# Performance work log

Hardware: AMD Instinct MI355X
Metric: run time of the kernel (lower is better)

## Reference

```python
import jax, jax.numpy as jnp
import numpy as np

D_MODEL = 1024
N_HEAD = 16
D_HEAD = D_MODEL // N_HEAD
EXP = 4
B, T = 2, 2048
EPS = 1e-5

def setup_inputs() -> dict:
    key = jax.random.key(0)
    ks = jax.random.split(key, 16)
    s = 0.02
    return {
        "x": jax.random.normal(ks[0], (B, T, D_MODEL), jnp.float32),
        "ln1_w": jnp.ones((D_MODEL,), jnp.float32),
        "ln1_b": jnp.zeros((D_MODEL,), jnp.float32),
        "attn_w": jax.random.normal(ks[1], (D_MODEL, 3 * D_MODEL), jnp.float32) * s,
        "attn_b": jnp.zeros((3 * D_MODEL,), jnp.float32),
        "proj_w": jax.random.normal(ks[2], (D_MODEL, D_MODEL), jnp.float32) * s,
        "proj_b": jnp.zeros((D_MODEL,), jnp.float32),
        "ln2_w": jnp.ones((D_MODEL,), jnp.float32),
        "ln2_b": jnp.zeros((D_MODEL,), jnp.float32),
        "fc_w": jax.random.normal(ks[3], (D_MODEL, EXP * D_MODEL), jnp.float32) * s,
        "fc_b": jnp.zeros((EXP * D_MODEL,), jnp.float32),
        "fc2_w": jax.random.normal(ks[4], (EXP * D_MODEL, D_MODEL), jnp.float32) * s,
        "fc2_b": jnp.zeros((D_MODEL,), jnp.float32),
    }

def _layernorm(x, w, b):
    mu = jnp.mean(x, axis=-1, keepdims=True)
    var = jnp.mean(jnp.square(x - mu), axis=-1, keepdims=True)
    return (x - mu) * jax.lax.rsqrt(var + EPS) * w + b

def _attn(x, attn_w, attn_b, proj_w, proj_b):
    Bx, Tx, C = x.shape
    qkv = x @ attn_w + attn_b  # [B,T,3C]
    q, k, v = jnp.split(qkv, 3, axis=-1)
    # [B, H, T, Dh]
    q = q.reshape(Bx, Tx, N_HEAD, D_HEAD).transpose(0, 2, 1, 3)
    k = k.reshape(Bx, Tx, N_HEAD, D_HEAD).transpose(0, 2, 1, 3)
    v = v.reshape(Bx, Tx, N_HEAD, D_HEAD).transpose(0, 2, 1, 3)
    att = jnp.einsum('bhqd,bhkd->bhqk', q, k) * (1.0 / np.sqrt(D_HEAD))
    causal = jnp.tril(jnp.ones((Tx, Tx), bool))
    att = jnp.where(causal, att, -jnp.inf)
    att = jax.nn.softmax(att, axis=-1)
    y = jnp.einsum('bhqk,bhkd->bhqd', att, v)
    y = y.transpose(0, 2, 1, 3).reshape(Bx, Tx, C)
    return y @ proj_w + proj_b

def reference(x, ln1_w, ln1_b, attn_w, attn_b, proj_w, proj_b,
              ln2_w, ln2_b, fc_w, fc_b, fc2_w, fc2_b):
    x = x + _attn(_layernorm(x, ln1_w, ln1_b), attn_w, attn_b, proj_w, proj_b)
    h = _layernorm(x, ln2_w, ln2_b)
    h = jax.nn.gelu(h @ fc_w + fc_b, approximate=False)  # exact GELU (torch nn.GELU default)
    x = x + (h @ fc2_w + fc2_b)
    return x
```

## Files before the change

### kernel.cpp

```cpp
#include <hip/hip_runtime.h>
#include <hip/hip_bf16.h>
#include <math.h>


#define D_MODEL 1024
#define N_HEAD  16
#define D_HEAD  64
#define SEQ_T   2048
#define BATCH   2
#define NROWS   (BATCH * SEQ_T)
#define C3      (3 * D_MODEL)
#define D_FF    (4 * D_MODEL)

typedef __bf16 bf16x8 __attribute__((ext_vector_type(8)));
typedef __bf16 bf16x4t __attribute__((ext_vector_type(4)));
typedef short  s16x4  __attribute__((ext_vector_type(4)));
typedef float  f32x4  __attribute__((ext_vector_type(4)));

#define WAIT_VM0() asm volatile("s_waitcnt vmcnt(0)" ::: "memory")
#define WAIT_VM2() asm volatile("s_waitcnt vmcnt(2)" ::: "memory")
#define WAIT_VM4() asm volatile("s_waitcnt vmcnt(4)" ::: "memory")
#define WAIT_VM6() asm volatile("s_waitcnt vmcnt(6)" ::: "memory")

__device__ __forceinline__ f32x4 mfma16_bf16(s16x4 a, s16x4 b, f32x4 c)
{
#if __has_builtin(__builtin_amdgcn_mfma_f32_16x16x16_bf16)
    return __builtin_amdgcn_mfma_f32_16x16x16_bf16(
        __builtin_bit_cast(bf16x4t, a), __builtin_bit_cast(bf16x4t, b), c, 0, 0, 0);
#else
    return __builtin_amdgcn_mfma_f32_16x16x16bf16_1k(a, b, c, 0, 0, 0);
#endif
}

__global__ __launch_bounds__(256) void ln_kernel(
    const float* __restrict__ in, const float* __restrict__ w,
    const float* __restrict__ b, __hip_bfloat16* __restrict__ out, int D)
{
    const int row = blockIdx.x;
    const int tid = threadIdx.x;
    const float* x = in + (size_t)row * 1024;

    const float4 v = *(const float4*)(x + tid * 4);
    float s  = v.x + v.y + v.z + v.w;
    float s2 = v.x * v.x + v.y * v.y + v.z * v.z + v.w * v.w;

    __shared__ float rs[256], rs2[256];
    rs[tid] = s; rs2[tid] = s2;
    __syncthreads();
    for (int off = 128; off > 0; off >>= 1) {
        if (tid < off) { rs[tid] += rs[tid + off]; rs2[tid] += rs2[tid + off]; }
        __syncthreads();
    }
    const float mu   = rs[0] * (1.0f / 1024.0f);
    const float var  = rs2[0] * (1.0f / 1024.0f) - mu * mu;
    const float rstd = rsqrtf(var + 1e-5f);

    const float4 w4 = *(const float4*)(w + tid * 4);
    const float4 b4 = *(const float4*)(b + tid * 4);
    float o[4] = {(v.x - mu) * rstd * w4.x + b4.x,
                  (v.y - mu) * rstd * w4.y + b4.y,
                  (v.z - mu) * rstd * w4.z + b4.z,
                  (v.w - mu) * rstd * w4.w + b4.w};
    ushort4 pk;
    { __hip_bfloat16 e0 = __float2bfloat16(o[0]); pk.x = *(unsigned short*)&e0;
      __hip_bfloat16 e1 = __float2bfloat16(o[1]); pk.y = *(unsigned short*)&e1;
      __hip_bfloat16 e2 = __float2bfloat16(o[2]); pk.z = *(unsigned short*)&e2;
      __hip_bfloat16 e3 = __float2bfloat16(o[3]); pk.w = *(unsigned short*)&e3; }
    *(ushort4*)(out + (size_t)row * 1024 + tid * 4) = pk;
}

__global__ __launch_bounds__(256) void prep_kernel(
    const float* __restrict__ attn_w, const float* __restrict__ proj_w,
    const float* __restrict__ fc_w,   const float* __restrict__ fc2_w,
    __hip_bfloat16* __restrict__ attn_wt, __hip_bfloat16* __restrict__ proj_wt,
    __hip_bfloat16* __restrict__ fc_wt,   __hip_bfloat16* __restrict__ fc2_wt,
    const float* __restrict__ x, const float* __restrict__ ln1_w,
    const float* __restrict__ ln1_b, __hip_bfloat16* __restrict__ ln_out)
{
    __shared__ float smem[32 * 33];
    int tb = blockIdx.x;
    const int tid = threadIdx.x;

    if (tb >= 12288) {
        const int row = tb - 12288;
        const float* xr = x + (size_t)row * 1024;
        const float4 v = *(const float4*)(xr + tid * 4);
        float s  = v.x + v.y + v.z + v.w;
        float s2 = v.x * v.x + v.y * v.y + v.z * v.z + v.w * v.w;
        float* rs  = smem;
        float* rs2 = smem + 256;
        rs[tid] = s; rs2[tid] = s2;
        __syncthreads();
        for (int off = 128; off > 0; off >>= 1) {
            if (tid < off) { rs[tid] += rs[tid + off]; rs2[tid] += rs2[tid + off]; }
            __syncthreads();
        }
        const float mu   = rs[0] * (1.0f / 1024.0f);
        const float var  = rs2[0] * (1.0f / 1024.0f) - mu * mu;
        const float rstd = rsqrtf(var + 1e-5f);
        const float4 w4 = *(const float4*)(ln1_w + tid * 4);
        const float4 b4 = *(const float4*)(ln1_b + tid * 4);
        float o[4] = {(v.x - mu) * rstd * w4.x + b4.x,
                      (v.y - mu) * rstd * w4.y + b4.y,
                      (v.z - mu) * rstd * w4.z + b4.z,
                      (v.w - mu) * rstd * w4.w + b4.w};
        ushort4 pk;
        { __hip_bfloat16 e0 = __float2bfloat16(o[0]); pk.x = *(unsigned short*)&e0;
          __hip_bfloat16 e1 = __float2bfloat16(o[1]); pk.y = *(unsigned short*)&e1;
          __hip_bfloat16 e2 = __float2bfloat16(o[2]); pk.z = *(unsigned short*)&e2;
          __hip_bfloat16 e3 = __float2bfloat16(o[3]); pk.w = *(unsigned short*)&e3; }
        *(ushort4*)(ln_out + (size_t)row * 1024 + tid * 4) = pk;
        return;
    }

    float (*t)[33] = (float(*)[33])smem;
    const float* W; __hip_bfloat16* Wt; int K, N;
    if (tb < 3072)      { W = attn_w; Wt = attn_wt; K = D_MODEL; N = C3; }
    else if (tb < 4096) { tb -= 3072; W = proj_w; Wt = proj_wt; K = D_MODEL; N = D_MODEL; }
    else if (tb < 8192) { tb -= 4096; W = fc_w;   Wt = fc_wt;   K = D_MODEL; N = D_FF; }
    else                { tb -= 8192; W = fc2_w;  Wt = fc2_wt;  K = D_FF;    N = D_MODEL; }
    const int ntx = N >> 5;
    const int k0 = (tb / ntx) * 32;
    const int n0 = (tb % ntx) * 32;

    const int row = tid >> 3;
    const int c4  = (tid & 7) * 4;

    const float4 v = *(const float4*)&W[(size_t)(k0 + row) * N + n0 + c4];
    t[row][c4 + 0] = v.x; t[row][c4 + 1] = v.y;
    t[row][c4 + 2] = v.z; t[row][c4 + 3] = v.w;
    __syncthreads();

    ushort4 pk;
    { __hip_bfloat16 e0 = __float2bfloat16(t[c4 + 0][row]); pk.x = *(unsigned short*)&e0;
      __hip_bfloat16 e1 = __float2bfloat16(t[c4 + 1][row]); pk.y = *(unsigned short*)&e1;
      __hip_bfloat16 e2 = __float2bfloat16(t[c4 + 2][row]); pk.z = *(unsigned short*)&e2;
      __hip_bfloat16 e3 = __float2bfloat16(t[c4 + 3][row]); pk.w = *(unsigned short*)&e3; }
    *(ushort4*)&Wt[(size_t)(n0 + row) * K + k0 + c4] = pk;
}

__device__ __forceinline__ void async16(const __hip_bfloat16* g, __hip_bfloat16* l)
{
    __builtin_amdgcn_global_load_lds(
        (const __attribute__((address_space(1))) void*)g,
        (__attribute__((address_space(3))) void*)l, 16, 0, 0);
}

__device__ __forceinline__ float gelu_fast(float v)
{
    const float t = v * (0.7978845608f + 0.0356774081f * v * v);
    return v / (1.0f + exp2f(-2.885390082f * t));
}

__device__ __forceinline__ void swz_xcd(int& bx, int& by)
{
    const int nbx = gridDim.x;
    const int nwg = nbx * gridDim.y;
    int lin = blockIdx.y * nbx + blockIdx.x;
    const int per = nwg >> 3;
    lin = (lin & 7) * per + (lin >> 3);
    bx = lin % nbx;
    by = lin / nbx;
}


__device__ __forceinline__ void gemm8p_core(
    const __hip_bfloat16* __restrict__ A,
    const __hip_bfloat16* __restrict__ Bt,
    int K, int row0, int col0, f32x4 (&acc)[8][4],
    __hip_bfloat16 (*Asl)[4][64 * 64], __hip_bfloat16 (*Bsl)[2][128 * 64])
{
    const int tid  = threadIdx.x;
    const int wv   = tid >> 6;
    const int lane = tid & 63;
    const int ln15 = lane & 15;
    const int lq   = lane >> 4;
    const int wr   = wv >> 2;
    const int wc   = wv & 3;

    const int srow = tid >> 3;
    const int sg   = ((tid & 7) ^ ((tid >> 3) & 7)) * 8;
    const __hip_bfloat16* Ab = A  + (size_t)(row0 + srow) * K + sg;
    const __hip_bfloat16* Bb = Bt + (size_t)(col0 + srow) * K + sg;
    const int nt = K >> 6;

#pragma unroll
    for (int mi = 0; mi < 8; ++mi)
#pragma unroll
        for (int ni = 0; ni < 4; ++ni) acc[mi][ni] = (f32x4){0.f, 0.f, 0.f, 0.f};

    auto stA = [&](int t, int buf, int b) {
        async16(Ab + (size_t)(b * 64) * K + t * 64, &Asl[buf][b][0] + tid * 8);
    };
    auto stB = [&](int t, int buf, int h) {
        async16(Bb + (size_t)(h * 128) * K + t * 64, &Bsl[buf][h][0] + tid * 8);
        async16(Bb + (size_t)(h * 128 + 64) * K + t * 64,
                &Bsl[buf][h][0] + 4096 + tid * 8);
    };

    const int rg0 = (lq ^ (ln15 & 7)) * 8;
    const int rg1 = ((4 | lq) ^ (ln15 & 7)) * 8;
    auto ldA = [&](int buf, int mi, int kk) -> bf16x8 {
        return *(const bf16x8*)&Asl[buf][wr * 2 + (mi >> 2)]
            [((mi & 3) * 16 + ln15) * 64 + (kk ? rg1 : rg0)];
    };
    auto ldB = [&](int buf, int ni, int kk) -> bf16x8 {
        return *(const bf16x8*)&Bsl[buf][wc >> 1]
            [((wc & 1) * 64 + ni * 16 + ln15) * 64 + (kk ? rg1 : rg0)];
    };

    stB(0, 0, 0); stB(0, 0, 1);
    stA(0, 0, 0); stA(0, 0, 2); stA(0, 0, 1); stA(0, 0, 3);
    WAIT_VM0();
    __builtin_amdgcn_s_barrier();

    for (int t = 0; t < nt; ++t) {
        const int pp = t & 1, op = pp ^ 1;
        const int tc = (t + 1 < nt) ? t + 1 : nt - 1;
        bf16x8 af[2][2], bfr[4][2];

#pragma unroll
        for (int m = 0; m < 2; ++m) { af[m][0] = ldA(pp, m, 0); af[m][1] = ldA(pp, m, 1); }
#pragma unroll
        for (int ni = 0; ni < 4; ++ni) { bfr[ni][0] = ldB(pp, ni, 0); bfr[ni][1] = ldB(pp, ni, 1); }
        stB(tc, op, 0);
        __builtin_amdgcn_s_barrier();
        __builtin_amdgcn_s_setprio(1);
#pragma unroll
        for (int kk = 0; kk < 2; ++kk)
#pragma unroll
            for (int m = 0; m < 2; ++m)
#pragma unroll
                for (int ni = 0; ni < 4; ++ni)
                    acc[m][ni] = __builtin_amdgcn_mfma_f32_16x16x32_bf16(
                        af[m][kk], bfr[ni][kk], acc[m][ni], 0, 0, 0);
        __builtin_amdgcn_s_setprio(0);
        __builtin_amdgcn_s_barrier();

#pragma unroll
        for (int m = 0; m < 2; ++m) { af[m][0] = ldA(pp, 2 + m, 0); af[m][1] = ldA(pp, 2 + m, 1); }
        stB(tc, op, 1);
        WAIT_VM4();
        __builtin_amdgcn_s_barrier();
        __builtin_amdgcn_s_setprio(1);
#pragma unroll
        for (int kk = 0; kk < 2; ++kk)
#pragma unroll
            for (int m = 0; m < 2; ++m)
#pragma unroll
                for (int ni = 0; ni < 4; ++ni)
                    acc[2 + m][ni] = __builtin_amdgcn_mfma_f32_16x16x32_bf16(
                        af[m][kk], bfr[ni][kk], acc[2 + m][ni], 0, 0, 0);
        __builtin_amdgcn_s_setprio(0);
        __builtin_amdgcn_s_barrier();

#pragma unroll
        for (int m = 0; m < 2; ++m) { af[m][0] = ldA(pp, 4 + m, 0); af[m][1] = ldA(pp, 4 + m, 1); }
        stA(tc, op, 0); stA(tc, op, 2);
        __builtin_amdgcn_s_barrier();
        __builtin_amdgcn_s_setprio(1);
#pragma unroll
        for (int kk = 0; kk < 2; ++kk)
#pragma unroll
            for (int m = 0; m < 2; ++m)
#pragma unroll
                for (int ni = 0; ni < 4; ++ni)
                    acc[4 + m][ni] = __builtin_amdgcn_mfma_f32_16x16x32_bf16(
                        af[m][kk], bfr[ni][kk], acc[4 + m][ni], 0, 0, 0);
        __builtin_amdgcn_s_setprio(0);
        __builtin_amdgcn_s_barrier();

#pragma unroll
        for (int m = 0; m < 2; ++m) { af[m][0] = ldA(pp, 6 + m, 0); af[m][1] = ldA(pp, 6 + m, 1); }
        stA(tc, op, 1); stA(tc, op, 3);
        WAIT_VM2();
        __builtin_amdgcn_s_barrier();
        __builtin_amdgcn_s_setprio(1);
#pragma unroll
        for (int kk = 0; kk < 2; ++kk)
#pragma unroll
            for (int m = 0; m < 2; ++m)
#pragma unroll
                for (int ni = 0; ni < 4; ++ni)
                    acc[6 + m][ni] = __builtin_amdgcn_mfma_f32_16x16x32_bf16(
                        af[m][kk], bfr[ni][kk], acc[6 + m][ni], 0, 0, 0);
        __builtin_amdgcn_s_setprio(0);
        __builtin_amdgcn_s_barrier();
    }
}

__global__ __launch_bounds__(512, 1) void gemm8p_kernel(
    const __hip_bfloat16* __restrict__ A,
    const __hip_bfloat16* __restrict__ Bt,
    const float* __restrict__ bias,
    __hip_bfloat16* __restrict__ Cout,
    int M, int N, int K, int act)
{
    __shared__ __align__(16) __hip_bfloat16 Asl[2][4][64 * 64];
    __shared__ __align__(16) __hip_bfloat16 Bsl[2][2][128 * 64];

    int bx, by;
    swz_xcd(bx, by);
    const int row0 = by * 256;
    const int col0 = bx * 256;

    f32x4 acc[8][4];
    gemm8p_core(A, Bt, K, row0, col0, acc, Asl, Bsl);

    const int tid  = threadIdx.x;
    const int wv   = tid >> 6;
    const int lane = tid & 63;
    const int ln15 = lane & 15;
    const int lq   = lane >> 4;
    const int mbase = (wv >> 2) * 128;
    const int nbase = (wv & 3) * 64;

#pragma unroll
    for (int mi = 0; mi < 8; ++mi) {
#pragma unroll
        for (int ni = 0; ni < 4; ++ni) {
            const int gc = col0 + nbase + ni * 16 + ln15;
            const float bv = bias[gc];
#pragma unroll
            for (int r = 0; r < 4; ++r) {
                const int gr = row0 + mbase + mi * 16 + lq * 4 + r;
                float v = acc[mi][ni][r] + bv;
                if (act == 1) v = gelu_fast(v);
                Cout[(size_t)gr * N + gc] = __float2bfloat16(v);
            }
        }
    }
}

__global__ __launch_bounds__(512, 1) void qkv8p_kernel(
    const __hip_bfloat16* __restrict__ A,
    const __hip_bfloat16* __restrict__ Bt,
    const float* __restrict__ bias,
    __hip_bfloat16* __restrict__ Qb,
    __hip_bfloat16* __restrict__ Kb,
    __hip_bfloat16* __restrict__ Vtb)
{
    __shared__ __align__(16) __hip_bfloat16 Asl[2][4][64 * 64];
    __shared__ __align__(16) __hip_bfloat16 Bsl[2][2][128 * 64];

    int bx, by;
    swz_xcd(bx, by);
    const int row0 = by * 256;
    const int col0 = bx * 256;

    f32x4 acc[8][4];
    gemm8p_core(A, Bt, D_MODEL, row0, col0, acc, Asl, Bsl);

    const int tid  = threadIdx.x;
    const int wv   = tid >> 6;
    const int lane = tid & 63;
    const int ln15 = lane & 15;
    const int lq   = lane >> 4;
    const int mbase = (wv >> 2) * 128;
    const int nbase = (wv & 3) * 64;

#pragma unroll
    for (int mi = 0; mi < 8; ++mi) {
        const int gr0 = row0 + mbase + mi * 16 + lq * 4;
        const int bb  = gr0 >> 11;
        const int q0  = gr0 & 2047;
#pragma unroll
        for (int ni = 0; ni < 4; ++ni) {
            const int gc  = col0 + nbase + ni * 16 + ln15;
            const float bv = bias[gc];
            const int sec = gc >> 10;
            const int hd  = (gc & 1023) >> 6;
            const int d   = gc & 63;
            if (sec == 2) {
                unsigned short u[4];
#pragma unroll
                for (int r = 0; r < 4; ++r) {
                    __hip_bfloat16 e = __float2bfloat16(acc[mi][ni][r] + bv);
                    u[r] = *(unsigned short*)&e;
                }
                uint2 pk;
                pk.x = (unsigned int)u[0] | ((unsigned int)u[1] << 16);
                pk.y = (unsigned int)u[2] | ((unsigned int)u[3] << 16);
                *(uint2*)(Vtb + ((size_t)((bb * N_HEAD + hd) * D_HEAD + d)) * SEQ_T + q0) = pk;
            } else {
                __hip_bfloat16* dst = (sec == 0 ? Qb : Kb)
                    + ((size_t)((bb * N_HEAD + hd) * SEQ_T + q0)) * D_HEAD + d;
#pragma unroll
                for (int r = 0; r < 4; ++r)
                    dst[(size_t)r * D_HEAD] = __float2bfloat16(acc[mi][ni][r] + bv);
            }
        }
    }
}

__device__ __forceinline__ void stage_db2w(
    const __hip_bfloat16* __restrict__ Ab, const __hip_bfloat16* __restrict__ Bb,
    int K, int kt, __hip_bfloat16* __restrict__ as,
    __hip_bfloat16* __restrict__ bs, int tid)
{
    const int k0 = kt * 64;
#pragma unroll
    for (int s = 0; s < 2; ++s) {
        async16(Ab + k0 + s * 32, as + s * 64 * 32 + tid * 8);
#pragma unroll
        for (int i = 0; i < 2; ++i)
            async16(Bb + (size_t)(i * 64) * K + k0 + s * 32,
                    bs + s * 128 * 32 + i * 64 * 32 + tid * 8);
    }
}

__device__ __forceinline__ void gemm_db2w(
    const __hip_bfloat16* __restrict__ A,
    const __hip_bfloat16* __restrict__ Bt,
    int K, int row0, int col0, f32x4 (&acc)[2][4])
{
    __shared__ __align__(16) __hip_bfloat16 Asl[3][2 * 64 * 32];
    __shared__ __align__(16) __hip_bfloat16 Bsl[3][2 * 128 * 32];

    const int tid  = threadIdx.x;
    const int wv   = tid >> 6;
    const int lane = tid & 63;
    const int ln15 = lane & 15;
    const int lq   = lane >> 4;
    const int mbase = (wv >> 1) * 32;
    const int nbase = (wv & 1) * 64;
    const int rcol = (lq ^ ((ln15 >> 1) & 3)) * 8;
    const int ssw  = ((tid & 3) ^ ((tid >> 3) & 3)) * 8;
    const __hip_bfloat16* Ab = A  + (size_t)(row0 + (tid >> 2)) * K + ssw;
    const __hip_bfloat16* Bb = Bt + (size_t)(col0 + (tid >> 2)) * K + ssw;
    const int nt = K >> 6;

#pragma unroll
    for (int mi = 0; mi < 2; ++mi)
#pragma unroll
        for (int ni = 0; ni < 4; ++ni) acc[mi][ni] = (f32x4){0.f, 0.f, 0.f, 0.f};

    stage_db2w(Ab, Bb, K, 0, &Asl[0][0], &Bsl[0][0], tid);
    stage_db2w(Ab, Bb, K, 1, &Asl[1][0], &Bsl[1][0], tid);
    WAIT_VM6();
    __builtin_amdgcn_s_barrier();

    for (int t = 0; t < nt; ++t) {
        const int p   = t % 3;
        const int p2  = (t + 2) % 3;
        const int tcl = (t + 2 < nt) ? t + 2 : nt - 1;
        bf16x8 af[2][2], bfr[2][4];

#pragma unroll
        for (int s = 0; s < 2; ++s) {
#pragma unroll
            for (int mi = 0; mi < 2; ++mi)
                af[s][mi] = *(const bf16x8*)
                    &Asl[p][s * 64 * 32 + (mbase + mi * 16 + ln15) * 32 + rcol];
#pragma unroll
            for (int ni = 0; ni < 4; ++ni)
                bfr[s][ni] = *(const bf16x8*)
                    &Bsl[p][s * 128 * 32 + (nbase + ni * 16 + ln15) * 32 + rcol];
        }

        stage_db2w(Ab, Bb, K, tcl, &Asl[p2][0], &Bsl[p2][0], tid);

        WAIT_VM6();
        __builtin_amdgcn_s_barrier();

        __builtin_amdgcn_s_setprio(1);
#pragma unroll
        for (int s = 0; s < 2; ++s)
#pragma unroll
            for (int mi = 0; mi < 2; ++mi)
#pragma unroll
                for (int ni = 0; ni < 4; ++ni)
                    acc[mi][ni] = __builtin_amdgcn_mfma_f32_16x16x32_bf16(
                        af[s][mi], bfr[s][ni], acc[mi][ni], 0, 0, 0);
        __builtin_amdgcn_s_setprio(0);
    }
}

__global__ __launch_bounds__(256, 2) void gemm64_kernel(
    const __hip_bfloat16* __restrict__ A,
    const __hip_bfloat16* __restrict__ Bt,
    const float* __restrict__ bias,
    const float* __restrict__ residual,
    void* __restrict__ Cout,
    int M, int N, int K, int act, int outBf16)
{
    int bx, by;
    swz_xcd(bx, by);
    const int row0 = by * 64;
    const int col0 = bx * 128;

    f32x4 acc[2][4];
    gemm_db2w(A, Bt, K, row0, col0, acc);

    const int tid  = threadIdx.x;
    const int wv   = tid >> 6;
    const int lane = tid & 63;
    const int ln15 = lane & 15;
    const int lq   = lane >> 4;
    const int mbase = (wv >> 1) * 32;
    const int nbase = (wv & 1) * 64;

#pragma unroll
    for (int mi = 0; mi < 2; ++mi) {
#pragma unroll
        for (int ni = 0; ni < 4; ++ni) {
            const int gc = col0 + nbase + ni * 16 + ln15;
            const float bv = bias[gc];
#pragma unroll
            for (int r = 0; r < 4; ++r) {
                const int gr = row0 + mbase + mi * 16 + lq * 4 + r;
                float v = acc[mi][ni][r] + bv;
                if (act == 1) v = gelu_fast(v);
                if (residual) v += residual[(size_t)gr * N + gc];
                if (outBf16)
                    ((__hip_bfloat16*)Cout)[(size_t)gr * N + gc] = __float2bfloat16(v);
                else
                    ((float*)Cout)[(size_t)gr * N + gc] = v;
            }
        }
    }
}

#define ATQ 64
#define ATK 128
#define NQT (SEQ_T / ATQ)
#define VP2 136

__global__ __launch_bounds__(256) void mfma_attn_kernel(
    const __hip_bfloat16* __restrict__ Qb,
    const __hip_bfloat16* __restrict__ Kb,
    const __hip_bfloat16* __restrict__ Vtb,
    __hip_bfloat16* __restrict__ y)
{
    __shared__ __align__(16) __hip_bfloat16 Ks[2][ATK * 64];
    __shared__ __align__(16) __hip_bfloat16 Vts[2][D_HEAD * VP2];

    const int flat = (blockIdx.z * gridDim.y + blockIdx.y) * gridDim.x + blockIdx.x;
    const int xcd  = flat & 7;
    const int slot = flat >> 3;
    const int pair = slot & 15;
    const int hb   = slot >> 4;
    const int h    = xcd + 8 * (hb & 1);
    const int b    = hb >> 1;

    const int tid  = threadIdx.x;
    const int wv   = tid >> 6;
    const int lane = tid & 63;
    const int ln15 = lane & 15;
    const int lq   = lane >> 4;

    const __hip_bfloat16* Qh = Qb  + (size_t)(b * N_HEAD + h) * SEQ_T * D_HEAD;
    const __hip_bfloat16* Kh = Kb  + (size_t)(b * N_HEAD + h) * SEQ_T * D_HEAD;
    const __hip_bfloat16* Vh = Vtb + (size_t)(b * N_HEAD + h) * D_HEAD * SEQ_T;
    const size_t bT = (size_t)b * SEQ_T;

    const float CEXP = 0.18033688011f;
    const float DTHR = 8.0f / CEXP;

    const int kr  = tid >> 3, kg = tid & 7;
    const int ksg = (kg ^ (kr & 7)) * 8;
    bf16x8 vreg[4];
    const int vr = tid >> 4, vc = tid & 15;

    auto issueK = [&](int kb, int buf) {
#pragma unroll
        for (int i = 0; i < 4; ++i)
            async16(Kh + (size_t)(kb + kr + i * 32) * D_HEAD + ksg,
                    &Ks[buf][i * 2048] + tid * 8);
    };
    auto issueV = [&](int kb) {
#pragma unroll
        for (int i = 0; i < 4; ++i)
            vreg[i] = *(const bf16x8*)(Vh + (size_t)(vr + i * 16) * SEQ_T + kb + vc * 8);
    };
    auto commitV = [&](int buf) {
#pragma unroll
        for (int i = 0; i < 4; ++i)
            *(bf16x8*)&Vts[buf][(vr + i * 16) * VP2 + vc * 8] = vreg[i];
    };

    const int rg0 = (lq ^ (ln15 & 7)) * 8;
    const int rg1 = ((4 | lq) ^ (ln15 & 7)) * 8;

#pragma unroll 1
    for (int half = 0; half < 2; ++half) {
        const int qt    = half == 0 ? pair : (NQT - 1 - pair);
        const int qbase = qt * ATQ;
        const int ntk   = (qt >> 1) + 1;
        const int qg    = qbase + wv * 16 + ln15;

        bf16x8 qf[2];
#pragma unroll
        for (int kc = 0; kc < 2; ++kc)
            qf[kc] = *(const bf16x8*)(Qh + (size_t)(qbase + wv * 16 + ln15) * D_HEAD
                                      + kc * 32 + lq * 8);

        f32x4 Oacc[4];
#pragma unroll
        for (int dn = 0; dn < 4; ++dn) Oacc[dn] = (f32x4){0.f, 0.f, 0.f, 0.f};
        float m_run = -INFINITY, l_run = 0.f;

        issueK(0, 0);
        issueV(0);

        for (int t = 0; t < ntk; ++t) {
            const int kb  = t * ATK;
            const int buf = t & 1;
            commitV(buf);
            __syncthreads();
            if (t + 1 < ntk) {
                issueK((t + 1) * ATK, buf ^ 1);
                issueV((t + 1) * ATK);
            }

            f32x4 st[8];
#pragma unroll
            for (int jf = 0; jf < 8; ++jf) st[jf] = (f32x4){0.f, 0.f, 0.f, 0.f};
            __builtin_amdgcn_s_setprio(1);
#pragma unroll
            for (int jf = 0; jf < 8; ++jf) {
                const int rw = jf * 16 + ln15;
                const bf16x8 kf0 = *(const bf16x8*)&Ks[buf][rw * 64 + rg0];
                const bf16x8 kf1 = *(const bf16x8*)&Ks[buf][rw * 64 + rg1];
                st[jf] = __builtin_amdgcn_mfma_f32_16x16x32_bf16(kf0, qf[0], st[jf], 0, 0, 0);
                st[jf] = __builtin_amdgcn_mfma_f32_16x16x32_bf16(kf1, qf[1], st[jf], 0, 0, 0);
            }
            __builtin_amdgcn_s_setprio(0);

            if (t == ntk - 1) {
#pragma unroll
                for (int jf = 0; jf < 8; ++jf)
#pragma unroll
                    for (int r = 0; r < 4; ++r)
                        if ((kb + jf * 16 + lq * 4 + r) > qg) st[jf][r] = -INFINITY;
            }

            float tm0 = st[0][0], tm1 = st[0][1], tm2 = st[0][2], tm3 = st[0][3];
#pragma unroll
            for (int jf = 1; jf < 8; ++jf) {
                tm0 = fmaxf(tm0, st[jf][0]);
                tm1 = fmaxf(tm1, st[jf][1]);
                tm2 = fmaxf(tm2, st[jf][2]);
                tm3 = fmaxf(tm3, st[jf][3]);
            }
            float tmax = fmaxf(fmaxf(tm0, tm1), fmaxf(tm2, tm3));
            tmax = fmaxf(tmax, __shfl_xor(tmax, 16));
            tmax = fmaxf(tmax, __shfl_xor(tmax, 32));

            if (!__all(tmax <= m_run + DTHR)) {
                const float mnew  = fmaxf(m_run, tmax);
                const float alpha = exp2f((m_run - mnew) * CEXP);
                l_run *= alpha;
                m_run = mnew;
                float a4[4];
#pragma unroll
                for (int r = 0; r < 4; ++r) a4[r] = __shfl(alpha, lq * 4 + r);
#pragma unroll
                for (int dn = 0; dn < 4; ++dn)
#pragma unroll
                    for (int r = 0; r < 4; ++r) Oacc[dn][r] *= a4[r];
            }
            const float mc = m_run * CEXP;
            float ps0 = 0.f, ps1 = 0.f, ps2 = 0.f, ps3 = 0.f;
#pragma unroll
            for (int jf = 0; jf < 8; ++jf) {
                const float p0 = exp2f(fmaf(st[jf][0], CEXP, -mc));
                const float p1 = exp2f(fmaf(st[jf][1], CEXP, -mc));
                const float p2 = exp2f(fmaf(st[jf][2], CEXP, -mc));
                const float p3 = exp2f(fmaf(st[jf][3], CEXP, -mc));
                st[jf][0] = p0; st[jf][1] = p1; st[jf][2] = p2; st[jf][3] = p3;
                ps0 += p0; ps1 += p1; ps2 += p2; ps3 += p3;
            }
            float psum = (ps0 + ps1) + (ps2 + ps3);
            psum += __shfl_xor(psum, 16);
            psum += __shfl_xor(psum, 32);
            l_run += psum;

            __builtin_amdgcn_s_setprio(1);
#pragma unroll
            for (int jf = 0; jf < 8; ++jf) {
                s16x4 pfr;
#pragma unroll
                for (int s = 0; s < 4; ++s) {
                    __hip_bfloat16 e = __float2bfloat16(st[jf][s]);
                    pfr[s] = __builtin_bit_cast(short, e);
                }
#pragma unroll
                for (int dn = 0; dn < 4; ++dn) {
                    const s16x4 vfr = *(const s16x4*)&Vts[buf][(dn * 16 + ln15) * VP2
                                                            + jf * 16 + lq * 4];
                    Oacc[dn] = mfma16_bf16(pfr, vfr, Oacc[dn]);
                }
            }
            __builtin_amdgcn_s_setprio(0);
        }

        __syncthreads();
        float il[4];
#pragma unroll
        for (int r = 0; r < 4; ++r) il[r] = 1.0f / __shfl(l_run, lq * 4 + r);
#pragma unroll
        for (int dn = 0; dn < 4; ++dn)
#pragma unroll
            for (int r = 0; r < 4; ++r)
                Ks[0][(wv * 16 + lq * 4 + r) * 72 + dn * 16 + ln15] =
                    __float2bfloat16(Oacc[dn][r] * il[r]);
        __syncthreads();
        const int r2 = lane >> 3, c8 = (lane & 7) * 8;
#pragma unroll
        for (int i = 0; i < 2; ++i) {
            const int row = wv * 16 + r2 + 8 * i;
            const bf16x8 val = *(const bf16x8*)&Ks[0][row * 72 + c8];
            *(bf16x8*)(y + (bT + qbase + row) * D_MODEL + h * D_HEAD + c8) = val;
        }
        __syncthreads();
    }
}

extern "C" void kernel_launch(void* const* d_in, const int* in_sizes, int n_in,
                              void* d_out, int out_size, void* d_ws, size_t ws_size,
                              hipStream_t stream)
{
    const float* x      = (const float*)d_in[0];
    const float* ln1_w  = (const float*)d_in[1];
    const float* ln1_b  = (const float*)d_in[2];
    const float* attn_w = (const float*)d_in[3];
    const float* attn_b = (const float*)d_in[4];
    const float* proj_w = (const float*)d_in[5];
    const float* proj_b = (const float*)d_in[6];
    const float* ln2_w  = (const float*)d_in[7];
    const float* ln2_b  = (const float*)d_in[8];
    const float* fc_w   = (const float*)d_in[9];
    const float* fc_b   = (const float*)d_in[10];
    const float* fc2_w  = (const float*)d_in[11];
    const float* fc2_b  = (const float*)d_in[12];
    float* out = (float*)d_out;

    char* ws = (char*)d_ws;
    __hip_bfloat16* Qb      = (__hip_bfloat16*)(ws);
    __hip_bfloat16* Kb      = (__hip_bfloat16*)(ws + (size_t)8  * 1024 * 1024);
    __hip_bfloat16* Vtb     = (__hip_bfloat16*)(ws + (size_t)16 * 1024 * 1024);
    __hip_bfloat16* h_bf    = (__hip_bfloat16*)(ws);
    __hip_bfloat16* ln_buf  = (__hip_bfloat16*)(ws + (size_t)32 * 1024 * 1024);
    __hip_bfloat16* y_buf   = (__hip_bfloat16*)(ws + (size_t)40 * 1024 * 1024);
    float*          xmid    = (float*)(ws + (size_t)48 * 1024 * 1024);
    __hip_bfloat16* attn_wt = (__hip_bfloat16*)(ws + (size_t)64 * 1024 * 1024);
    __hip_bfloat16* proj_wt = (__hip_bfloat16*)(ws + (size_t)70 * 1024 * 1024);
    __hip_bfloat16* fc_wt   = (__hip_bfloat16*)(ws + (size_t)72 * 1024 * 1024);
    __hip_bfloat16* fc2_wt  = (__hip_bfloat16*)(ws + (size_t)80 * 1024 * 1024);

    dim3 blk256(256);
    dim3 blk512(512);

    prep_kernel<<<dim3(12288 + NROWS), blk256, 0, stream>>>(
        attn_w, proj_w, fc_w, fc2_w, attn_wt, proj_wt, fc_wt, fc2_wt,
        x, ln1_w, ln1_b, ln_buf);

    qkv8p_kernel<<<dim3(C3 / 256, NROWS / 256), blk512, 0, stream>>>(
        ln_buf, attn_wt, attn_b, Qb, Kb, Vtb);

    mfma_attn_kernel<<<dim3(NQT / 2, N_HEAD, BATCH), blk256, 0, stream>>>(
        Qb, Kb, Vtb, y_buf);

    gemm64_kernel<<<dim3(D_MODEL / 128, NROWS / 64), blk256, 0, stream>>>(
        y_buf, proj_wt, proj_b, x, xmid, NROWS, D_MODEL, D_MODEL, 0, 0);

    ln_kernel<<<dim3(NROWS), blk256, 0, stream>>>(xmid, ln2_w, ln2_b, ln_buf, D_MODEL);

    gemm8p_kernel<<<dim3(D_FF / 256, NROWS / 256), blk512, 0, stream>>>(
        ln_buf, fc_wt, fc_b, h_bf, NROWS, D_FF, D_MODEL, 1);

    gemm64_kernel<<<dim3(D_MODEL / 128, NROWS / 64), blk256, 0, stream>>>(
        h_bf, fc2_wt, fc2_b, xmid, out, NROWS, D_MODEL, D_FF, 0, 0);
}
```

Baseline: 334.8 us.

## Process both paired causal query tiles concurrently in one 512-thread attention block

The attention kernel previously handled its two paired query tiles (a short one and a long one) one after the other with 256 threads. It now uses 512 threads, where the first 256 take the short tile and the second 256 take the long tile. Both groups share one K/V stream out of shared memory, and the short group simply idles once its keys run out. This halves the K/V loads per pair and doubles the parallelism per block, but the short-tile warps idle during the later iterations and the larger block may reduce occupancy.

Result: slower. 349.9 us (+4.5%).

```diff
diff --git a/kernel.cpp b/kernel.cpp
--- a/kernel.cpp
+++ b/kernel.cpp
@@ -526,7 +526,7 @@
 #define NQT (SEQ_T / ATQ)
 #define VP2 136
 
-__global__ __launch_bounds__(256) void mfma_attn_kernel(
+__global__ __launch_bounds__(512, 2) void mfma_attn_kernel(
     const __hip_bfloat16* __restrict__ Qb,
     const __hip_bfloat16* __restrict__ Kb,
     const __hip_bfloat16* __restrict__ Vtb,
@@ -544,7 +544,8 @@
     const int b    = hb >> 1;
 
     const int tid  = threadIdx.x;
-    const int wv   = tid >> 6;
+    const int wq   = tid >> 8;
+    const int wv4  = (tid >> 6) & 3;
     const int lane = tid & 63;
     const int ln15 = lane & 15;
     const int lq   = lane >> 4;
@@ -557,62 +558,61 @@
     const float CEXP = 0.18033688011f;
     const float DTHR = 8.0f / CEXP;
 
-    const int kr  = tid >> 3, kg = tid & 7;
-    const int ksg = (kg ^ (kr & 7)) * 8;
-    bf16x8 vreg[4];
+    const int qt_me  = (wq == 0) ? pair : (NQT - 1 - pair);
+    const int qbase  = qt_me * ATQ;
+    const int ntk_me = (qt_me >> 1) + 1;
+    const int ntkMax = ((NQT - 1 - pair) >> 1) + 1;
+    const int qg     = qbase + wv4 * 16 + ln15;
+
+    const int ksg = ((tid & 7) ^ ((tid >> 3) & 7)) * 8;
+    bf16x8 vreg[2];
     const int vr = tid >> 4, vc = tid & 15;
 
     auto issueK = [&](int kb, int buf) {
 #pragma unroll
-        for (int i = 0; i < 4; ++i)
-            async16(Kh + (size_t)(kb + kr + i * 32) * D_HEAD + ksg,
-                    &Ks[buf][i * 2048] + tid * 8);
+        for (int i = 0; i < 2; ++i)
+            async16(Kh + (size_t)(kb + (tid >> 3) + i * 64) * D_HEAD + ksg,
+                    &Ks[buf][i * 4096] + tid * 8);
     };
     auto issueV = [&](int kb) {
 #pragma unroll
-        for (int i = 0; i < 4; ++i)
-            vreg[i] = *(const bf16x8*)(Vh + (size_t)(vr + i * 16) * SEQ_T + kb + vc * 8);
+        for (int i = 0; i < 2; ++i)
+            vreg[i] = *(const bf16x8*)(Vh + (size_t)(vr + i * 32) * SEQ_T + kb + vc * 8);
     };
     auto commitV = [&](int buf) {
 #pragma unroll
-        for (int i = 0; i < 4; ++i)
-            *(bf16x8*)&Vts[buf][(vr + i * 16) * VP2 + vc * 8] = vreg[i];
+        for (int i = 0; i < 2; ++i)
+            *(bf16x8*)&Vts[buf][(vr + i * 32) * VP2 + vc * 8] = vreg[i];
     };
 
     const int rg0 = (lq ^ (ln15 & 7)) * 8;
     const int rg1 = ((4 | lq) ^ (ln15 & 7)) * 8;
 
-#pragma unroll 1
-    for (int half = 0; half < 2; ++half) {
-        const int qt    = half == 0 ? pair : (NQT - 1 - pair);
-        const int qbase = qt * ATQ;
-        const int ntk   = (qt >> 1) + 1;
-        const int qg    = qbase + wv * 16 + ln15;
-
-        bf16x8 qf[2];
-#pragma unroll
-        for (int kc = 0; kc < 2; ++kc)
-            qf[kc] = *(const bf16x8*)(Qh + (size_t)(qbase + wv * 16 + ln15) * D_HEAD
-                                      + kc * 32 + lq * 8);
-
-        f32x4 Oacc[4];
-#pragma unroll
-        for (int dn = 0; dn < 4; ++dn) Oacc[dn] = (f32x4){0.f, 0.f, 0.f, 0.f};
-        float m_run = -INFINITY, l_run = 0.f;
-
-        issueK(0, 0);
-        issueV(0);
-
-        for (int t = 0; t < ntk; ++t) {
-            const int kb  = t * ATK;
-            const int buf = t & 1;
-            commitV(buf);
-            __syncthreads();
-            if (t + 1 < ntk) {
-                issueK((t + 1) * ATK, buf ^ 1);
-                issueV((t + 1) * ATK);
-            }
-
+    bf16x8 qf[2];
+#pragma unroll
+    for (int kc = 0; kc < 2; ++kc)
+        qf[kc] = *(const bf16x8*)(Qh + (size_t)(qbase + wv4 * 16 + ln15) * D_HEAD
+                                  + kc * 32 + lq * 8);
+
+    f32x4 Oacc[4];
+#pragma unroll
+    for (int dn = 0; dn < 4; ++dn) Oacc[dn] = (f32x4){0.f, 0.f, 0.f, 0.f};
+    float m_run = -INFINITY, l_run = 0.f;
+
+    issueK(0, 0);
+    issueV(0);
+
+    for (int t = 0; t < ntkMax; ++t) {
+        const int kb  = t * ATK;
+        const int buf = t & 1;
+        commitV(buf);
+        __syncthreads();
+        if (t + 1 < ntkMax) {
+            issueK((t + 1) * ATK, buf ^ 1);
+            issueV((t + 1) * ATK);
+        }
+
+        if (t < ntk_me) {
             f32x4 st[8];
 #pragma unroll
             for (int jf = 0; jf < 8; ++jf) st[jf] = (f32x4){0.f, 0.f, 0.f, 0.f};
@@ -627,7 +627,7 @@
             }
             __builtin_amdgcn_s_setprio(0);
 
-            if (t == ntk - 1) {
+            if (t == ntk_me - 1) {
 #pragma unroll
                 for (int jf = 0; jf < 8; ++jf)
 #pragma unroll
@@ -694,26 +694,25 @@
             }
             __builtin_amdgcn_s_setprio(0);
         }
-
-        __syncthreads();
-        float il[4];
-#pragma unroll
-        for (int r = 0; r < 4; ++r) il[r] = 1.0f / __shfl(l_run, lq * 4 + r);
-#pragma unroll
-        for (int dn = 0; dn < 4; ++dn)
-#pragma unroll
-            for (int r = 0; r < 4; ++r)
-                Ks[0][(wv * 16 + lq * 4 + r) * 72 + dn * 16 + ln15] =
-                    __float2bfloat16(Oacc[dn][r] * il[r]);
-        __syncthreads();
-        const int r2 = lane >> 3, c8 = (lane & 7) * 8;
-#pragma unroll
-        for (int i = 0; i < 2; ++i) {
-            const int row = wv * 16 + r2 + 8 * i;
-            const bf16x8 val = *(const bf16x8*)&Ks[0][row * 72 + c8];
-            *(bf16x8*)(y + (bT + qbase + row) * D_MODEL + h * D_HEAD + c8) = val;
-        }
-        __syncthreads();
+    }
+
+    __syncthreads();
+    float il[4];
+#pragma unroll
+    for (int r = 0; r < 4; ++r) il[r] = 1.0f / __shfl(l_run, lq * 4 + r);
+#pragma unroll
+    for (int dn = 0; dn < 4; ++dn)
+#pragma unroll
+        for (int r = 0; r < 4; ++r)
+            Ks[wq][(wv4 * 16 + lq * 4 + r) * 72 + dn * 16 + ln15] =
+                __float2bfloat16(Oacc[dn][r] * il[r]);
+    __syncthreads();
+    const int r2 = lane >> 3, c8 = (lane & 7) * 8;
+#pragma unroll
+    for (int i = 0; i < 2; ++i) {
+        const int row = wv4 * 16 + r2 + 8 * i;
+        const bf16x8 val = *(const bf16x8*)&Ks[wq][row * 72 + c8];
+        *(bf16x8*)(y + (bT + qbase + row) * D_MODEL + h * D_HEAD + c8) = val;
     }
 }
 
@@ -759,7 +758,7 @@
     qkv8p_kernel<<<dim3(C3 / 256, NROWS / 256), blk512, 0, stream>>>(
         ln_buf, attn_wt, attn_b, Qb, Kb, Vtb);
 
-    mfma_attn_kernel<<<dim3(NQT / 2, N_HEAD, BATCH), blk256, 0, stream>>>(
+    mfma_attn_kernel<<<dim3(NQT / 2, N_HEAD, BATCH), blk512, 0, stream>>>(
         Qb, Kb, Vtb, y_buf);
 
     gemm64_kernel<<<dim3(D_MODEL / 128, NROWS / 64), blk256, 0, stream>>>(
```
